# Kernel tuning notes

Measured on AMD Instinct MI355X. Metric: run time of the kernel, lower is better.

Reference implementation:

```python
import jax, jax.numpy as jnp
import numpy as np

N_NODES = 50000
N_EDGES = 800000
IN_CH = 256
OUT_CH = 128
HID = 2 * OUT_CH  # 256
N_GRAPHS = 64


def setup_inputs() -> dict:
    key = jax.random.key(0)
    k = jax.random.split(key, 8)
    x = jax.random.normal(k[0], (N_NODES, IN_CH), dtype=jnp.float32)
    edge_index = jax.random.randint(k[1], (2, N_EDGES), 0, N_NODES, dtype=jnp.int64)
    batch = jnp.sort(jax.random.randint(k[2], (N_NODES,), 0, N_GRAPHS, dtype=jnp.int64))
    # GCNConv parameters (glorot-ish init)
    W1 = jax.random.normal(k[3], (IN_CH, HID), dtype=jnp.float32) / np.sqrt(IN_CH)
    b1 = jnp.zeros((HID,), dtype=jnp.float32)
    W2 = jax.random.normal(k[4], (HID, OUT_CH), dtype=jnp.float32) / np.sqrt(HID)
    b2 = jnp.zeros((OUT_CH,), dtype=jnp.float32)
    return {"x": x, "W1": W1, "b1": b1, "W2": W2, "b2": b2,
            "edge_index": edge_index, "batch": batch}


def _gcn_conv(x, W, b, src, dst, n):
    """PyG GCNConv: transform, then sym-normalized aggregation with self-loops."""
    h = x @ W  # [N, F_out]
    # degree over destination nodes, including the added self-loop
    deg = jnp.zeros((n,), dtype=h.dtype).at[dst].add(1.0) + 1.0
    dinv = jax.lax.rsqrt(deg)
    norm = dinv[src] * dinv[dst]            # [E]
    agg = jnp.zeros_like(h).at[dst].add(h[src] * norm[:, None])
    agg = agg + h * (1.0 / deg)[:, None]    # self-loop contribution: deg_i^{-1}
    return agg + b


def reference(x, W1, b1, W2, b2, edge_index, batch):
    src, dst = edge_index[0], edge_index[1]
    # dropout is identity in eval mode (training=False)
    h = jax.nn.elu(_gcn_conv(x, W1, b1, src, dst, N_NODES))
    h = _gcn_conv(h, W2, b2, src, dst, N_NODES)
    # global mean pool over graphs
    ones = jnp.ones((N_NODES,), dtype=h.dtype)
    counts = jax.ops.segment_sum(ones, batch, num_segments=N_GRAPHS)
    sums = jax.ops.segment_sum(h, batch, num_segments=N_GRAPHS)
    return sums / jnp.maximum(counts, 1.0)[:, None]
```

## Files before the change

### kernel.cpp

```cpp
#include <hip/hip_runtime.h>
#include <hip/hip_bf16.h>

#define N_NODES 50000
#define N_EDGES 800000
#define IN_CH 256
#define HID 256
#define OUT_CH 128
#define N_GRAPHS 64
#define SCAN_BLOCKS 196
#define M_PAD 50048
#define POOL_CHUNK 32
#define POOL_BLOCKS ((N_NODES + POOL_CHUNK - 1) / POOL_CHUNK)

typedef __bf16 bf16x8 __attribute__((ext_vector_type(8)));
typedef float f32x4 __attribute__((ext_vector_type(4)));
typedef unsigned short u16x8 __attribute__((ext_vector_type(8)));

__device__ __forceinline__ float bf2f(unsigned short u) {
    union { unsigned int i; float f; } x; x.i = ((unsigned int)u) << 16; return x.f;
}
__device__ __forceinline__ unsigned short f2bf(float f) {
    union { float f; unsigned int i; } x; x.f = f;
    unsigned int r = x.i + 0x7FFFu + ((x.i >> 16) & 1u);
    return (unsigned short)(r >> 16);
}

__device__ __forceinline__ void load16(const void* g, void* l) {
    __builtin_amdgcn_global_load_lds(
        (const __attribute__((address_space(1))) void*)g,
        (__attribute__((address_space(3))) void*)l, 16, 0, 0);
}

__global__ __launch_bounds__(256) void count_kernel(const int* __restrict__ ei,
                                                    int* __restrict__ cnt) {
    int e = blockIdx.x * 256 + threadIdx.x;
    if (e < N_EDGES) atomicAdd(&cnt[ei[N_EDGES + e]], 1);
}

__global__ __launch_bounds__(256) void scan_a_kernel(const int* __restrict__ cnt,
                                                     int* __restrict__ rowptr,
                                                     int* __restrict__ blocksum,
                                                     float* __restrict__ dinv,
                                                     float* __restrict__ invdeg) {
    __shared__ int tmp[256];
    int t = threadIdx.x;
    int i = blockIdx.x * 256 + t;
    int v = (i < N_NODES) ? cnt[i] : 0;
    int x = v;
    tmp[t] = x;
    __syncthreads();
#pragma unroll
    for (int off = 1; off < 256; off <<= 1) {
        int y = (t >= off) ? tmp[t - off] : 0;
        __syncthreads();
        x += y;
        tmp[t] = x;
        __syncthreads();
    }
    if (i < N_NODES) {
        rowptr[i] = x - v;
        float d = (float)v + 1.0f;
        dinv[i] = rsqrtf(d);
        invdeg[i] = 1.0f / d;
    }
    if (t == 255) blocksum[blockIdx.x] = x;
}

__global__ __launch_bounds__(256) void scan_b_kernel(const int* __restrict__ blocksum,
                                                     int* __restrict__ blockoff,
                                                     int* __restrict__ rowptr) {
    __shared__ int tmp[256];
    int t = threadIdx.x;
    int v = (t < SCAN_BLOCKS) ? blocksum[t] : 0;
    int x = v;
    tmp[t] = x;
    __syncthreads();
#pragma unroll
    for (int off = 1; off < 256; off <<= 1) {
        int y = (t >= off) ? tmp[t - off] : 0;
        __syncthreads();
        x += y;
        tmp[t] = x;
        __syncthreads();
    }
    if (t < SCAN_BLOCKS) blockoff[t] = x - v;
    if (t == 255) rowptr[N_NODES] = x;
}

__global__ __launch_bounds__(256) void scan_c_kernel(int* __restrict__ rowptr,
                                                     const int* __restrict__ blockoff) {
    int i = blockIdx.x * 256 + threadIdx.x;
    if (i < N_NODES) rowptr[i] += blockoff[blockIdx.x];
}

__global__ __launch_bounds__(256) void fill_kernel(const int* __restrict__ ei,
                                                   const int* __restrict__ rowptr,
                                                   int* __restrict__ fillp,
                                                   int2* __restrict__ edge2,
                                                   const float* __restrict__ dinv) {
    int e = blockIdx.x * 256 + threadIdx.x;
    if (e >= N_EDGES) return;
    int s = ei[e];
    int d = ei[N_EDGES + e];
    int p = rowptr[d] + atomicAdd(&fillp[d], 1);
    float w = dinv[s] * dinv[d];
    edge2[p] = make_int2(s, __float_as_int(w));
}

__global__ __launch_bounds__(256) void cvt_w_kernel(const float* __restrict__ W1,
                                                    const float* __restrict__ W2,
                                                    unsigned short* __restrict__ w1t,
                                                    unsigned short* __restrict__ w2t) {
    int i = blockIdx.x * 256 + threadIdx.x;
    if (i < HID * IN_CH) {
        int n = i >> 8, k = i & 255;
        w1t[i] = f2bf(W1[k * HID + n]);
    } else if (i < HID * IN_CH + OUT_CH * HID) {
        int j = i - HID * IN_CH;
        int n = j >> 8, k = j & 255;
        w2t[j] = f2bf(W2[k * OUT_CH + n]);
    }
}

__global__ __launch_bounds__(256) void gemm_mfma_kernel(
        const unsigned short* __restrict__ A,
        const unsigned short* __restrict__ Bt,
        unsigned short* __restrict__ C,
        int N) {
    const int K = 256;
    __shared__ char As[8192];
    __shared__ char Bs[8192];
    int tid = threadIdx.x;
    int bm = blockIdx.x * 128;
    int bn = blockIdx.y * 128;
    int lane = tid & 63, wave = tid >> 6;
    int lane15 = lane & 15, quad = lane >> 4;
    int wm0 = (wave >> 1) << 6;
    int wn0 = (wave & 1) << 6;

    int s1 = tid, s2 = tid + 256;
    int r1 = s1 >> 2, q1 = (s1 & 3) ^ ((r1 >> 1) & 3);
    int r2 = s2 >> 2, q2 = (s2 & 3) ^ ((r2 >> 1) & 3);
    const char* gA1 = (const char*)(A + (size_t)(bm + r1) * K) + (q1 << 4);
    const char* gA2 = (const char*)(A + (size_t)(bm + r2) * K) + (q2 << 4);
    const char* gB1 = (const char*)(Bt + (size_t)(bn + r1) * K) + (q1 << 4);
    const char* gB2 = (const char*)(Bt + (size_t)(bn + r2) * K) + (q2 << 4);
    char* lA1 = As + (wave << 10);
    char* lA2 = As + 4096 + (wave << 10);
    char* lB1 = Bs + (wave << 10);
    char* lB2 = Bs + 4096 + (wave << 10);

    int swm = (lane15 >> 1) & 3;
    f32x4 acc[4][4];
#pragma unroll
    for (int mt = 0; mt < 4; mt++)
#pragma unroll
        for (int nt = 0; nt < 4; nt++)
            acc[mt][nt] = (f32x4){0.f, 0.f, 0.f, 0.f};

    for (int k0 = 0; k0 < K; k0 += 32) {
        __syncthreads();
        load16(gA1 + (k0 << 1), lA1);
        load16(gA2 + (k0 << 1), lA2);
        load16(gB1 + (k0 << 1), lB1);
        load16(gB2 + (k0 << 1), lB2);
        __syncthreads();
        bf16x8 af[4], bfr[4];
#pragma unroll
        for (int t = 0; t < 4; t++) {
            int ra = wm0 + t * 16 + lane15;
            af[t] = *(const bf16x8*)(As + ra * 64 + ((quad ^ swm) << 4));
            int rb = wn0 + t * 16 + lane15;
            bfr[t] = *(const bf16x8*)(Bs + rb * 64 + ((quad ^ swm) << 4));
        }
#pragma unroll
        for (int mt = 0; mt < 4; mt++)
#pragma unroll
            for (int nt = 0; nt < 4; nt++)
                acc[mt][nt] = __builtin_amdgcn_mfma_f32_16x16x32_bf16(
                    af[mt], bfr[nt], acc[mt][nt], 0, 0, 0);
    }

#pragma unroll
    for (int mt = 0; mt < 4; mt++) {
        int rowb = bm + wm0 + mt * 16 + quad * 4;
#pragma unroll
        for (int nt = 0; nt < 4; nt++) {
            int col = bn + wn0 + nt * 16 + lane15;
            f32x4 a = acc[mt][nt];
            C[(size_t)(rowb + 0) * N + col] = f2bf(a[0]);
            C[(size_t)(rowb + 1) * N + col] = f2bf(a[1]);
            C[(size_t)(rowb + 2) * N + col] = f2bf(a[2]);
            C[(size_t)(rowb + 3) * N + col] = f2bf(a[3]);
        }
    }
}

__global__ __launch_bounds__(256) void gemm_mfma_x_kernel(
        const float* __restrict__ A,
        const unsigned short* __restrict__ Bt,
        unsigned short* __restrict__ C,
        int N) {
    const int K = 256;
    __shared__ char As[8192];
    __shared__ char Bs[8192];
    int tid = threadIdx.x;
    int bm = blockIdx.x * 128;
    int bn = blockIdx.y * 128;
    int lane = tid & 63, wave = tid >> 6;
    int lane15 = lane & 15, quad = lane >> 4;
    int wm0 = (wave >> 1) << 6;
    int wn0 = (wave & 1) << 6;

    int s1 = tid, s2 = tid + 256;
    int r1 = s1 >> 2, q1 = (s1 & 3) ^ ((r1 >> 1) & 3);
    int r2 = s2 >> 2, q2 = (s2 & 3) ^ ((r2 >> 1) & 3);
    const bool in1 = (bm + r1) < N_NODES;
    const bool in2 = (bm + r2) < N_NODES;
    const float* gA1 = A + (size_t)(bm + r1) * K + (q1 << 3);
    const float* gA2 = A + (size_t)(bm + r2) * K + (q2 << 3);
    const char* gB1 = (const char*)(Bt + (size_t)(bn + r1) * K) + (q1 << 4);
    const char* gB2 = (const char*)(Bt + (size_t)(bn + r2) * K) + (q2 << 4);
    char* lB1 = Bs + (wave << 10);
    char* lB2 = Bs + 4096 + (wave << 10);

    int swm = (lane15 >> 1) & 3;
    f32x4 acc[4][4];
#pragma unroll
    for (int mt = 0; mt < 4; mt++)
#pragma unroll
        for (int nt = 0; nt < 4; nt++)
            acc[mt][nt] = (f32x4){0.f, 0.f, 0.f, 0.f};

    const float4 z4 = make_float4(0.f, 0.f, 0.f, 0.f);
    for (int k0 = 0; k0 < K; k0 += 32) {
        __syncthreads();
        load16(gB1 + (k0 << 1), lB1);
        load16(gB2 + (k0 << 1), lB2);
        float4 a0 = in1 ? *(const float4*)(gA1 + k0)     : z4;
        float4 a1 = in1 ? *(const float4*)(gA1 + k0 + 4) : z4;
        float4 a2 = in2 ? *(const float4*)(gA2 + k0)     : z4;
        float4 a3 = in2 ? *(const float4*)(gA2 + k0 + 4) : z4;
        u16x8 u1 = { f2bf(a0.x), f2bf(a0.y), f2bf(a0.z), f2bf(a0.w),
                     f2bf(a1.x), f2bf(a1.y), f2bf(a1.z), f2bf(a1.w) };
        u16x8 u2 = { f2bf(a2.x), f2bf(a2.y), f2bf(a2.z), f2bf(a2.w),
                     f2bf(a3.x), f2bf(a3.y), f2bf(a3.z), f2bf(a3.w) };
        *(u16x8*)(As + s1 * 16) = u1;
        *(u16x8*)(As + s2 * 16) = u2;
        __syncthreads();
        bf16x8 af[4], bfr[4];
#pragma unroll
        for (int t = 0; t < 4; t++) {
            int ra = wm0 + t * 16 + lane15;
            af[t] = *(const bf16x8*)(As + ra * 64 + ((quad ^ swm) << 4));
            int rb = wn0 + t * 16 + lane15;
            bfr[t] = *(const bf16x8*)(Bs + rb * 64 + ((quad ^ swm) << 4));
        }
#pragma unroll
        for (int mt = 0; mt < 4; mt++)
#pragma unroll
            for (int nt = 0; nt < 4; nt++)
                acc[mt][nt] = __builtin_amdgcn_mfma_f32_16x16x32_bf16(
                    af[mt], bfr[nt], acc[mt][nt], 0, 0, 0);
    }

#pragma unroll
    for (int mt = 0; mt < 4; mt++) {
        int rowb = bm + wm0 + mt * 16 + quad * 4;
#pragma unroll
        for (int nt = 0; nt < 4; nt++) {
            int col = bn + wn0 + nt * 16 + lane15;
            f32x4 a = acc[mt][nt];
            C[(size_t)(rowb + 0) * N + col] = f2bf(a[0]);
            C[(size_t)(rowb + 1) * N + col] = f2bf(a[1]);
            C[(size_t)(rowb + 2) * N + col] = f2bf(a[2]);
            C[(size_t)(rowb + 3) * N + col] = f2bf(a[3]);
        }
    }
}

#define ACC4(V, W) \
    acc.x += bf2f(V.x) * W; acc.y += bf2f(V.y) * W; \
    acc.z += bf2f(V.z) * W; acc.w += bf2f(V.w) * W;

__global__ __launch_bounds__(256) void agg1_kernel(const unsigned short* __restrict__ h,
                                                   const float* __restrict__ bias,
                                                   const int* __restrict__ rowptr,
                                                   const int2* __restrict__ edge2,
                                                   const float* __restrict__ invdeg,
                                                   unsigned short* __restrict__ out) {
    int node = blockIdx.x * 4 + (threadIdx.x >> 6);
    if (node >= N_NODES) return;
    int lane = threadIdx.x & 63;
    const ushort4* h4 = (const ushort4*)h;
    float id = invdeg[node];
    ushort4 sv = h4[(size_t)node * 64 + lane];
    float4 acc = make_float4(bf2f(sv.x) * id, bf2f(sv.y) * id,
                             bf2f(sv.z) * id, bf2f(sv.w) * id);
    int e0 = rowptr[node], e1 = rowptr[node + 1];
    int e = e0;
    for (; e + 7 < e1; e += 8) {
        int2 ed[8];
        ushort4 v[8];
#pragma unroll
        for (int j = 0; j < 8; j++) ed[j] = edge2[e + j];
#pragma unroll
        for (int j = 0; j < 8; j++) v[j] = h4[(size_t)ed[j].x * 64 + lane];
#pragma unroll
        for (int j = 0; j < 8; j++) {
            float w = __int_as_float(ed[j].y);
            ACC4(v[j], w);
        }
    }
    for (; e + 3 < e1; e += 4) {
        int2 ed[4];
        ushort4 v[4];
#pragma unroll
        for (int j = 0; j < 4; j++) ed[j] = edge2[e + j];
#pragma unroll
        for (int j = 0; j < 4; j++) v[j] = h4[(size_t)ed[j].x * 64 + lane];
#pragma unroll
        for (int j = 0; j < 4; j++) {
            float w = __int_as_float(ed[j].y);
            ACC4(v[j], w);
        }
    }
    for (; e < e1; e++) {
        int2 ed0 = edge2[e];
        float w0 = __int_as_float(ed0.y);
        ushort4 v0 = h4[(size_t)ed0.x * 64 + lane];
        ACC4(v0, w0);
    }
    float4 bb = ((const float4*)bias)[lane];
    acc.x += bb.x; acc.y += bb.y; acc.z += bb.z; acc.w += bb.w;
    acc.x = acc.x > 0.f ? acc.x : expm1f(acc.x);
    acc.y = acc.y > 0.f ? acc.y : expm1f(acc.y);
    acc.z = acc.z > 0.f ? acc.z : expm1f(acc.z);
    acc.w = acc.w > 0.f ? acc.w : expm1f(acc.w);
    ushort4 o;
    o.x = f2bf(acc.x); o.y = f2bf(acc.y); o.z = f2bf(acc.z); o.w = f2bf(acc.w);
    ((ushort4*)out)[(size_t)node * 64 + lane] = o;
}

#define ACC2(V, W) \
    acc.x += bf2f(V.x) * W; acc.y += bf2f(V.y) * W;

__global__ __launch_bounds__(256) void agg2_kernel(const unsigned short* __restrict__ h,
                                                   const float* __restrict__ bias,
                                                   const int* __restrict__ rowptr,
                                                   const int2* __restrict__ edge2,
                                                   const float* __restrict__ invdeg,
                                                   unsigned short* __restrict__ out) {
    int node = blockIdx.x * 4 + (threadIdx.x >> 6);
    if (node >= N_NODES) return;
    int lane = threadIdx.x & 63;
    const ushort2* h2 = (const ushort2*)h;
    float id = invdeg[node];
    ushort2 sv = h2[(size_t)node * 64 + lane];
    float2 acc = make_float2(bf2f(sv.x) * id, bf2f(sv.y) * id);
    int e0 = rowptr[node], e1 = rowptr[node + 1];
    int e = e0;
    for (; e + 7 < e1; e += 8) {
        int2 ed[8];
        ushort2 v[8];
#pragma unroll
        for (int j = 0; j < 8; j++) ed[j] = edge2[e + j];
#pragma unroll
        for (int j = 0; j < 8; j++) v[j] = h2[(size_t)ed[j].x * 64 + lane];
#pragma unroll
        for (int j = 0; j < 8; j++) {
            float w = __int_as_float(ed[j].y);
            ACC2(v[j], w);
        }
    }
    for (; e + 3 < e1; e += 4) {
        int2 ed[4];
        ushort2 v[4];
#pragma unroll
        for (int j = 0; j < 4; j++) ed[j] = edge2[e + j];
#pragma unroll
        for (int j = 0; j < 4; j++) v[j] = h2[(size_t)ed[j].x * 64 + lane];
#pragma unroll
        for (int j = 0; j < 4; j++) {
            float w = __int_as_float(ed[j].y);
            ACC2(v[j], w);
        }
    }
    for (; e < e1; e++) {
        int2 ed0 = edge2[e];
        float w0 = __int_as_float(ed0.y);
        ushort2 v0 = h2[(size_t)ed0.x * 64 + lane];
        ACC2(v0, w0);
    }
    float2 bb = ((const float2*)bias)[lane];
    acc.x += bb.x; acc.y += bb.y;
    ushort2 o;
    o.x = f2bf(acc.x); o.y = f2bf(acc.y);
    ((ushort2*)out)[(size_t)node * 64 + lane] = o;
}

__global__ __launch_bounds__(128) void pool_kernel(const unsigned short* __restrict__ h,
                                                   const int* __restrict__ batch,
                                                   float* __restrict__ pool,
                                                   float* __restrict__ gcnt) {
    int c = threadIdx.x;
    int n0 = blockIdx.x * POOL_CHUNK;
    int n1 = n0 + POOL_CHUNK;
    if (n1 > N_NODES) n1 = N_NODES;
    if (n0 >= N_NODES) return;
    float run = 0.f, cnt = 0.f;
    int g = batch[n0];
    for (int n = n0; n < n1; n++) {
        int gn = batch[n];
        if (gn != g) {
            atomicAdd(&pool[g * OUT_CH + c], run);
            if (c == 0) atomicAdd(&gcnt[g], cnt);
            run = 0.f; cnt = 0.f; g = gn;
        }
        run += bf2f(h[(size_t)n * OUT_CH + c]);
        if (c == 0) cnt += 1.f;
    }
    atomicAdd(&pool[g * OUT_CH + c], run);
    if (c == 0) atomicAdd(&gcnt[g], cnt);
}

__global__ __launch_bounds__(256) void final_kernel(const float* __restrict__ pool,
                                                    const float* __restrict__ gcnt,
                                                    float* __restrict__ out) {
    int i = blockIdx.x * 256 + threadIdx.x;
    if (i < N_GRAPHS * OUT_CH)
        out[i] = pool[i] / fmaxf(gcnt[i >> 7], 1.0f);
}

extern "C" void kernel_launch(void* const* d_in, const int* in_sizes, int n_in,
                              void* d_out, int out_size, void* d_ws, size_t ws_size,
                              hipStream_t stream) {
    const float* x  = (const float*)d_in[0];
    const float* W1 = (const float*)d_in[1];
    const float* b1 = (const float*)d_in[2];
    const float* W2 = (const float*)d_in[3];
    const float* b2 = (const float*)d_in[4];
    const int*   ei = (const int*)d_in[5];
    const int*   batch = (const int*)d_in[6];
    float* out = (float*)d_out;

    unsigned short* h1b = (unsigned short*)d_ws;
    unsigned short* hBb = h1b + (size_t)M_PAD * HID;
    unsigned short* h2b = hBb + (size_t)M_PAD * HID;
    unsigned short* w1t = h2b + (size_t)M_PAD * OUT_CH;
    unsigned short* w2t = w1t + HID * IN_CH;
    unsigned short* hcb = h1b;
    float* dinv   = (float*)(w2t + OUT_CH * HID);
    float* invdeg = dinv + N_NODES;
    int*   rowptr = (int*)(invdeg + N_NODES);
    int2*  edge2  = (int2*)(rowptr + 50016);
    int*   cnt    = (int*)(edge2 + N_EDGES);
    int*   fillp  = cnt + N_NODES;
    float* gcnt   = (float*)(fillp + N_NODES);
    float* pool   = gcnt + N_GRAPHS;
    int*   blocksum = (int*)(pool + N_GRAPHS * OUT_CH);
    int*   blockoff = blocksum + 256;

    size_t zbytes = ((size_t)N_NODES * 2 + N_GRAPHS + (size_t)N_GRAPHS * OUT_CH) * 4;
    hipMemsetAsync(cnt, 0, zbytes, stream);

    count_kernel<<<(N_EDGES + 255) / 256, 256, 0, stream>>>(ei, cnt);
    scan_a_kernel<<<SCAN_BLOCKS, 256, 0, stream>>>(cnt, rowptr, blocksum, dinv, invdeg);
    scan_b_kernel<<<1, 256, 0, stream>>>(blocksum, blockoff, rowptr);
    scan_c_kernel<<<SCAN_BLOCKS, 256, 0, stream>>>(rowptr, blockoff);
    fill_kernel<<<(N_EDGES + 255) / 256, 256, 0, stream>>>(ei, rowptr, fillp, edge2, dinv);

    cvt_w_kernel<<<(HID * IN_CH + OUT_CH * HID + 255) / 256, 256, 0, stream>>>(W1, W2, w1t, w2t);

    dim3 g1(M_PAD / 128, HID / 128);
    gemm_mfma_x_kernel<<<g1, 256, 0, stream>>>(x, w1t, h1b, HID);
    agg1_kernel<<<(N_NODES + 3) / 4, 256, 0, stream>>>(h1b, b1, rowptr, edge2, invdeg, hBb);

    dim3 g2(M_PAD / 128, OUT_CH / 128);
    gemm_mfma_kernel<<<g2, 256, 0, stream>>>(hBb, w2t, h2b, OUT_CH);
    agg2_kernel<<<(N_NODES + 3) / 4, 256, 0, stream>>>(h2b, b2, rowptr, edge2, invdeg, hcb);

    pool_kernel<<<POOL_BLOCKS, 128, 0, stream>>>(hcb, batch, pool, gcnt);
    final_kernel<<<(N_GRAPHS * OUT_CH + 255) / 256, 256, 0, stream>>>(pool, gcnt, out);
}
```

Measured before the change: 334.6 us.

## Split layer-1 features into column planes and drop scan fixup kernel

The first GEMM writes its output as two 128-column planes, and agg1 runs separate blocks per plane so each gather reads half-width rows and a smaller working set stays cache-resident. Row pointers are now computed as a per-block local prefix plus a block offset, which removes the scan_c pass. The block-offset scan is merged with the weight conversion kernel, cutting launches. In exchange, agg1 reads the edge list twice and does an extra offset lookup per row pointer.

```diff
diff --git a/kernel.cpp b/kernel.cpp
--- a/kernel.cpp
+++ b/kernel.cpp
@@ -11,6 +11,7 @@
 #define M_PAD 50048
 #define POOL_CHUNK 32
 #define POOL_BLOCKS ((N_NODES + POOL_CHUNK - 1) / POOL_CHUNK)
+#define AGG1_HALF 12500
 
 typedef __bf16 bf16x8 __attribute__((ext_vector_type(8)));
 typedef float f32x4 __attribute__((ext_vector_type(4)));
@@ -31,6 +32,11 @@
         (__attribute__((address_space(3))) void*)l, 16, 0, 0);
 }
 
+__device__ __forceinline__ int rp(const int* __restrict__ rl,
+                                  const int* __restrict__ boff, int i) {
+    return rl[i] + boff[i >> 8];
+}
+
 __global__ __launch_bounds__(256) void count_kernel(const int* __restrict__ ei,
                                                     int* __restrict__ cnt) {
     int e = blockIdx.x * 256 + threadIdx.x;
@@ -38,7 +44,7 @@
 }
 
 __global__ __launch_bounds__(256) void scan_a_kernel(const int* __restrict__ cnt,
-                                                     int* __restrict__ rowptr,
+                                                     int* __restrict__ rl,
                                                      int* __restrict__ blocksum,
                                                      float* __restrict__ dinv,
                                                      float* __restrict__ invdeg) {
@@ -57,8 +63,8 @@
         tmp[t] = x;
         __syncthreads();
     }
+    if (i <= N_NODES) rl[i] = x - v;
     if (i < N_NODES) {
-        rowptr[i] = x - v;
         float d = (float)v + 1.0f;
         dinv[i] = rsqrtf(d);
         invdeg[i] = 1.0f / d;
@@ -66,11 +72,24 @@
     if (t == 255) blocksum[blockIdx.x] = x;
 }
 
-__global__ __launch_bounds__(256) void scan_b_kernel(const int* __restrict__ blocksum,
-                                                     int* __restrict__ blockoff,
-                                                     int* __restrict__ rowptr) {
+__global__ __launch_bounds__(256) void scanb_cvtw_kernel(
+        const int* __restrict__ blocksum, int* __restrict__ blockoff,
+        const float* __restrict__ W1, const float* __restrict__ W2,
+        unsigned short* __restrict__ w1t, unsigned short* __restrict__ w2t) {
+    int t = threadIdx.x;
+    if (blockIdx.x < 384) {
+        int i = blockIdx.x * 256 + t;
+        if (i < HID * IN_CH) {
+            int n = i >> 8, k = i & 255;
+            w1t[i] = f2bf(W1[k * HID + n]);
+        } else {
+            int j = i - HID * IN_CH;
+            int n = j >> 8, k = j & 255;
+            w2t[j] = f2bf(W2[k * OUT_CH + n]);
+        }
+        return;
+    }
     __shared__ int tmp[256];
-    int t = threadIdx.x;
     int v = (t < SCAN_BLOCKS) ? blocksum[t] : 0;
     int x = v;
     tmp[t] = x;
@@ -84,17 +103,11 @@
         __syncthreads();
     }
     if (t < SCAN_BLOCKS) blockoff[t] = x - v;
-    if (t == 255) rowptr[N_NODES] = x;
-}
-
-__global__ __launch_bounds__(256) void scan_c_kernel(int* __restrict__ rowptr,
-                                                     const int* __restrict__ blockoff) {
-    int i = blockIdx.x * 256 + threadIdx.x;
-    if (i < N_NODES) rowptr[i] += blockoff[blockIdx.x];
 }
 
 __global__ __launch_bounds__(256) void fill_kernel(const int* __restrict__ ei,
-                                                   const int* __restrict__ rowptr,
+                                                   const int* __restrict__ rl,
+                                                   const int* __restrict__ boff,
                                                    int* __restrict__ fillp,
                                                    int2* __restrict__ edge2,
                                                    const float* __restrict__ dinv) {
@@ -102,24 +115,9 @@
     if (e >= N_EDGES) return;
     int s = ei[e];
     int d = ei[N_EDGES + e];
-    int p = rowptr[d] + atomicAdd(&fillp[d], 1);
+    int p = rp(rl, boff, d) + atomicAdd(&fillp[d], 1);
     float w = dinv[s] * dinv[d];
     edge2[p] = make_int2(s, __float_as_int(w));
-}
-
-__global__ __launch_bounds__(256) void cvt_w_kernel(const float* __restrict__ W1,
-                                                    const float* __restrict__ W2,
-                                                    unsigned short* __restrict__ w1t,
-                                                    unsigned short* __restrict__ w2t) {
-    int i = blockIdx.x * 256 + threadIdx.x;
-    if (i < HID * IN_CH) {
-        int n = i >> 8, k = i & 255;
-        w1t[i] = f2bf(W1[k * HID + n]);
-    } else if (i < HID * IN_CH + OUT_CH * HID) {
-        int j = i - HID * IN_CH;
-        int n = j >> 8, k = j & 255;
-        w2t[j] = f2bf(W2[k * OUT_CH + n]);
-    }
 }
 
 __global__ __launch_bounds__(256) void gemm_mfma_kernel(
@@ -199,8 +197,8 @@
 __global__ __launch_bounds__(256) void gemm_mfma_x_kernel(
         const float* __restrict__ A,
         const unsigned short* __restrict__ Bt,
-        unsigned short* __restrict__ C,
-        int N) {
+        unsigned short* __restrict__ Ca,
+        unsigned short* __restrict__ Cb) {
     const int K = 256;
     __shared__ char As[8192];
     __shared__ char Bs[8192];
@@ -269,85 +267,86 @@
         int rowb = bm + wm0 + mt * 16 + quad * 4;
 #pragma unroll
         for (int nt = 0; nt < 4; nt++) {
-            int col = bn + wn0 + nt * 16 + lane15;
+            int gc = bn + wn0 + nt * 16 + lane15;
+            unsigned short* Cp = (gc & 128) ? Cb : Ca;
+            int pc = gc & 127;
             f32x4 a = acc[mt][nt];
-            C[(size_t)(rowb + 0) * N + col] = f2bf(a[0]);
-            C[(size_t)(rowb + 1) * N + col] = f2bf(a[1]);
-            C[(size_t)(rowb + 2) * N + col] = f2bf(a[2]);
-            C[(size_t)(rowb + 3) * N + col] = f2bf(a[3]);
-        }
-    }
-}
-
-#define ACC4(V, W) \
-    acc.x += bf2f(V.x) * W; acc.y += bf2f(V.y) * W; \
-    acc.z += bf2f(V.z) * W; acc.w += bf2f(V.w) * W;
-
-__global__ __launch_bounds__(256) void agg1_kernel(const unsigned short* __restrict__ h,
+            Cp[(size_t)(rowb + 0) * 128 + pc] = f2bf(a[0]);
+            Cp[(size_t)(rowb + 1) * 128 + pc] = f2bf(a[1]);
+            Cp[(size_t)(rowb + 2) * 128 + pc] = f2bf(a[2]);
+            Cp[(size_t)(rowb + 3) * 128 + pc] = f2bf(a[3]);
+        }
+    }
+}
+
+#define ACC2(V, W) \
+    acc.x += bf2f(V.x) * W; acc.y += bf2f(V.y) * W;
+
+__global__ __launch_bounds__(256) void agg1_kernel(const unsigned short* __restrict__ h1a,
+                                                   const unsigned short* __restrict__ h1b,
                                                    const float* __restrict__ bias,
-                                                   const int* __restrict__ rowptr,
+                                                   const int* __restrict__ rl,
+                                                   const int* __restrict__ boff,
                                                    const int2* __restrict__ edge2,
                                                    const float* __restrict__ invdeg,
                                                    unsigned short* __restrict__ out) {
-    int node = blockIdx.x * 4 + (threadIdx.x >> 6);
-    if (node >= N_NODES) return;
+    int bx = blockIdx.x;
+    int plane = (bx >= AGG1_HALF) ? 1 : 0;
+    int node = (plane ? bx - AGG1_HALF : bx) * 4 + (threadIdx.x >> 6);
     int lane = threadIdx.x & 63;
-    const ushort4* h4 = (const ushort4*)h;
+    const ushort2* hp = (const ushort2*)(plane ? h1b : h1a);
+    int co = plane << 7;
     float id = invdeg[node];
-    ushort4 sv = h4[(size_t)node * 64 + lane];
-    float4 acc = make_float4(bf2f(sv.x) * id, bf2f(sv.y) * id,
-                             bf2f(sv.z) * id, bf2f(sv.w) * id);
-    int e0 = rowptr[node], e1 = rowptr[node + 1];
+    ushort2 sv = hp[(size_t)node * 64 + lane];
+    float2 acc = make_float2(bf2f(sv.x) * id, bf2f(sv.y) * id);
+    int e0 = rp(rl, boff, node);
+    int e1 = rp(rl, boff, node + 1);
     int e = e0;
     for (; e + 7 < e1; e += 8) {
         int2 ed[8];
-        ushort4 v[8];
+        ushort2 v[8];
 #pragma unroll
         for (int j = 0; j < 8; j++) ed[j] = edge2[e + j];
 #pragma unroll
-        for (int j = 0; j < 8; j++) v[j] = h4[(size_t)ed[j].x * 64 + lane];
+        for (int j = 0; j < 8; j++) v[j] = hp[(size_t)ed[j].x * 64 + lane];
 #pragma unroll
         for (int j = 0; j < 8; j++) {
             float w = __int_as_float(ed[j].y);
-            ACC4(v[j], w);
+            ACC2(v[j], w);
         }
     }
     for (; e + 3 < e1; e += 4) {
         int2 ed[4];
-        ushort4 v[4];
+        ushort2 v[4];
 #pragma unroll
         for (int j = 0; j < 4; j++) ed[j] = edge2[e + j];
 #pragma unroll
-        for (int j = 0; j < 4; j++) v[j] = h4[(size_t)ed[j].x * 64 + lane];
+        for (int j = 0; j < 4; j++) v[j] = hp[(size_t)ed[j].x * 64 + lane];
 #pragma unroll
         for (int j = 0; j < 4; j++) {
             float w = __int_as_float(ed[j].y);
-            ACC4(v[j], w);
+            ACC2(v[j], w);
         }
     }
     for (; e < e1; e++) {
         int2 ed0 = edge2[e];
         float w0 = __int_as_float(ed0.y);
-        ushort4 v0 = h4[(size_t)ed0.x * 64 + lane];
-        ACC4(v0, w0);
-    }
-    float4 bb = ((const float4*)bias)[lane];
-    acc.x += bb.x; acc.y += bb.y; acc.z += bb.z; acc.w += bb.w;
+        ushort2 v0 = hp[(size_t)ed0.x * 64 + lane];
+        ACC2(v0, w0);
+    }
+    float2 bb = ((const float2*)(bias + co))[lane];
+    acc.x += bb.x; acc.y += bb.y;
     acc.x = acc.x > 0.f ? acc.x : expm1f(acc.x);
     acc.y = acc.y > 0.f ? acc.y : expm1f(acc.y);
-    acc.z = acc.z > 0.f ? acc.z : expm1f(acc.z);
-    acc.w = acc.w > 0.f ? acc.w : expm1f(acc.w);
-    ushort4 o;
-    o.x = f2bf(acc.x); o.y = f2bf(acc.y); o.z = f2bf(acc.z); o.w = f2bf(acc.w);
-    ((ushort4*)out)[(size_t)node * 64 + lane] = o;
-}
-
-#define ACC2(V, W) \
-    acc.x += bf2f(V.x) * W; acc.y += bf2f(V.y) * W;
+    ushort2 o;
+    o.x = f2bf(acc.x); o.y = f2bf(acc.y);
+    ((ushort2*)(out + (size_t)node * 256 + co))[lane] = o;
+}
 
 __global__ __launch_bounds__(256) void agg2_kernel(const unsigned short* __restrict__ h,
                                                    const float* __restrict__ bias,
-                                                   const int* __restrict__ rowptr,
+                                                   const int* __restrict__ rl,
+                                                   const int* __restrict__ boff,
                                                    const int2* __restrict__ edge2,
                                                    const float* __restrict__ invdeg,
                                                    unsigned short* __restrict__ out) {
@@ -358,7 +357,8 @@
     float id = invdeg[node];
     ushort2 sv = h2[(size_t)node * 64 + lane];
     float2 acc = make_float2(bf2f(sv.x) * id, bf2f(sv.y) * id);
-    int e0 = rowptr[node], e1 = rowptr[node + 1];
+    int e0 = rp(rl, boff, node);
+    int e1 = rp(rl, boff, node + 1);
     int e = e0;
     for (; e + 7 < e1; e += 8) {
         int2 ed[8];
@@ -444,16 +444,17 @@
     const int*   batch = (const int*)d_in[6];
     float* out = (float*)d_out;
 
-    unsigned short* h1b = (unsigned short*)d_ws;
-    unsigned short* hBb = h1b + (size_t)M_PAD * HID;
+    unsigned short* h1a = (unsigned short*)d_ws;
+    unsigned short* h1b = h1a + (size_t)M_PAD * 128;
+    unsigned short* hBb = h1b + (size_t)M_PAD * 128;
     unsigned short* h2b = hBb + (size_t)M_PAD * HID;
     unsigned short* w1t = h2b + (size_t)M_PAD * OUT_CH;
     unsigned short* w2t = w1t + HID * IN_CH;
-    unsigned short* hcb = h1b;
+    unsigned short* hcb = h1a;
     float* dinv   = (float*)(w2t + OUT_CH * HID);
     float* invdeg = dinv + N_NODES;
-    int*   rowptr = (int*)(invdeg + N_NODES);
-    int2*  edge2  = (int2*)(rowptr + 50016);
+    int*   rl     = (int*)(invdeg + N_NODES);
+    int2*  edge2  = (int2*)(rl + 50016);
     int*   cnt    = (int*)(edge2 + N_EDGES);
     int*   fillp  = cnt + N_NODES;
     float* gcnt   = (float*)(fillp + N_NODES);
@@ -465,20 +466,19 @@
     hipMemsetAsync(cnt, 0, zbytes, stream);
 
     count_kernel<<<(N_EDGES + 255) / 256, 256, 0, stream>>>(ei, cnt);
-    scan_a_kernel<<<SCAN_BLOCKS, 256, 0, stream>>>(cnt, rowptr, blocksum, dinv, invdeg);
-    scan_b_kernel<<<1, 256, 0, stream>>>(blocksum, blockoff, rowptr);
-    scan_c_kernel<<<SCAN_BLOCKS, 256, 0, stream>>>(rowptr, blockoff);
-    fill_kernel<<<(N_EDGES + 255) / 256, 256, 0, stream>>>(ei, rowptr, fillp, edge2, dinv);
-
-    cvt_w_kernel<<<(HID * IN_CH + OUT_CH * HID + 255) / 256, 256, 0, stream>>>(W1, W2, w1t, w2t);
+    scan_a_kernel<<<SCAN_BLOCKS, 256, 0, stream>>>(cnt, rl, blocksum, dinv, invdeg);
+    scanb_cvtw_kernel<<<385, 256, 0, stream>>>(blocksum, blockoff, W1, W2, w1t, w2t);
+    fill_kernel<<<(N_EDGES + 255) / 256, 256, 0, stream>>>(ei, rl, blockoff, fillp, edge2, dinv);
 
     dim3 g1(M_PAD / 128, HID / 128);
-    gemm_mfma_x_kernel<<<g1, 256, 0, stream>>>(x, w1t, h1b, HID);
-    agg1_kernel<<<(N_NODES + 3) / 4, 256, 0, stream>>>(h1b, b1, rowptr, edge2, invdeg, hBb);
+    gemm_mfma_x_kernel<<<g1, 256, 0, stream>>>(x, w1t, h1a, h1b);
+    agg1_kernel<<<2 * AGG1_HALF, 256, 0, stream>>>(h1a, h1b, b1, rl, blockoff,
+                                                   edge2, invdeg, hBb);
 
     dim3 g2(M_PAD / 128, OUT_CH / 128);
     gemm_mfma_kernel<<<g2, 256, 0, stream>>>(hBb, w2t, h2b, OUT_CH);
-    agg2_kernel<<<(N_NODES + 3) / 4, 256, 0, stream>>>(h2b, b2, rowptr, edge2, invdeg, hcb);
+    agg2_kernel<<<(N_NODES + 3) / 4, 256, 0, stream>>>(h2b, b2, rl, blockoff,
+                                                       edge2, invdeg, hcb);
 
     pool_kernel<<<POOL_BLOCKS, 128, 0, stream>>>(hcb, batch, pool, gcnt);
     final_kernel<<<(N_GRAPHS * OUT_CH + 255) / 256, 256, 0, stream>>>(pool, gcnt, out);
```

Result: no change. 339.0 us (+1.3%).
